# Kernel optimization log

Hardware: AMD Instinct MI355X
Metric: run time of the kernel (lower is better)

The kernel has to match this reference:

```python
import jax, jax.numpy as jnp
import numpy as np

N, D_IN, D_LAT, K = 65536, 1024, 128, 512


def setup_inputs() -> dict:
    key = jax.random.key(0)
    k1, k2, k3 = jax.random.split(key, 3)
    x = jax.random.normal(k1, (N, D_IN), dtype=jnp.float32)
    W = jax.random.normal(k2, (D_IN, D_LAT), dtype=jnp.float32) * 0.02
    b = jnp.zeros((D_LAT,), dtype=jnp.float32)
    centroids = jax.random.normal(k3, (K, D_LAT), dtype=jnp.float32)
    return {"x": x, "W": W, "b": b, "centroids": centroids}


def reference(x, W, b, centroids):
    alpha = 1.0
    # encoder: single linear layer -> latent l [N, D_LAT]
    l = x @ W + b
    # dist_to_centroids: vectorized squared-Euclidean cdist [N, K]
    # ||l - c||^2 = ||l||^2 + ||c||^2 - 2 l.c
    D = (jnp.sum(l * l, axis=1, keepdims=True)
         + jnp.sum(centroids * centroids, axis=1)
         - 2.0 * (l @ centroids.T))
    # Student's t-distribution kernel
    num = jnp.power(1.0 + D / alpha, -(alpha + 1.0) / 2.0)
    Q = num / jnp.sum(num, axis=1, keepdims=True)
    # target distribution
    Fq = jnp.sum(Q, axis=0)            # [K]
    num2 = (Q * Q) / Fq                # [N, K]
    P = num2 / jnp.sum(num2, axis=1, keepdims=True)
    return (l, Q, P)
```

## Files before the change

kernel.cpp:

```cpp
#include <hip/hip_runtime.h>

#define NROWS 65536
#define DIN   1024
#define DLAT  128
#define KC    512

typedef __attribute__((ext_vector_type(8))) short bf16x8;
typedef __attribute__((ext_vector_type(4))) float f32x4;

#define GLDS16(gp, lp)                                                          \
    __builtin_amdgcn_global_load_lds((const __attribute__((address_space(1))) void*)(gp), \
                                     (__attribute__((address_space(3))) void*)(lp), 16, 0, 0)

__device__ inline short f2bf(float f) {
    unsigned u = __float_as_uint(f);
    return (short)((u + 0x7FFFu + ((u >> 16) & 1u)) >> 16);
}

__global__ __launch_bounds__(256) void prep_convert(const float* __restrict__ W,
                                                    const float* __restrict__ C,
                                                    short* __restrict__ Wt,
                                                    short* __restrict__ cb) {
    int idx = blockIdx.x * 256 + threadIdx.x;
    if (idx < DLAT * DIN) {
        int n = idx >> 10, k = idx & 1023;
        Wt[idx] = f2bf(W[k * DLAT + n]);
    } else {
        int i2 = idx - DLAT * DIN;
        if (i2 < KC * DLAT) cb[i2] = f2bf(C[i2]);
    }
}

__global__ __launch_bounds__(64) void prep_csq(const float* __restrict__ C,
                                               float* __restrict__ csq) {
    int row = blockIdx.x;
    int lane = threadIdx.x;
    float a = C[row * DLAT + lane];
    float b = C[row * DLAT + 64 + lane];
    float s = a * a + b * b;
    #pragma unroll
    for (int m = 32; m >= 1; m >>= 1) s += __shfl_xor(s, m, 64);
    if (lane == 0) csq[row] = s;
}

__global__ __launch_bounds__(256, 2) void fused_aq(const float* __restrict__ x,
                                                   const short* __restrict__ Wt,
                                                   const float* __restrict__ bias,
                                                   const short* __restrict__ cb,
                                                   const float* __restrict__ csq,
                                                   float* __restrict__ lout,
                                                   float* __restrict__ Qout,
                                                   float* __restrict__ partial) {
    __shared__ char lds[65536];
    const int t = threadIdx.x;
    const int wid = t >> 6, lane = t & 63;
    const int l16 = lane & 15, lhi = lane >> 4;
    const int row0 = blockIdx.x * 64;

    const float* xsrc = x + (long)(row0 + (t >> 4)) * DIN + (((t & 15) ^ ((t >> 4) & 15)) << 2);
    const short* wsrc = Wt + (long)(t >> 3) * DIN + (((t & 7) ^ ((t >> 3) & 7)) << 3);
    const int lofs = t * 16;

    f32x4 acc[8];
    #pragma unroll
    for (int i = 0; i < 8; ++i) acc[i] = (f32x4){0.f, 0.f, 0.f, 0.f};

    {
        char* xb = lds;
        char* wb = lds + 16384;
        #pragma unroll
        for (int j = 0; j < 4; ++j) {
            GLDS16(xsrc + j * 16 * DIN, xb + lofs + j * 4096);
            GLDS16(wsrc + j * 32 * DIN, wb + lofs + j * 4096);
        }
    }
    __syncthreads();

    int cur = 0;
    const int arow = wid * 16 + l16;
    for (int kc = 0; kc < 16; ++kc) {
        if (kc < 15) {
            char* xb = lds + (cur ^ 1) * 32768;
            char* wb = xb + 16384;
            const float* xp = xsrc + (kc + 1) * 64;
            const short* wp = wsrc + (kc + 1) * 64;
            #pragma unroll
            for (int j = 0; j < 4; ++j) {
                GLDS16(xp + j * 16 * DIN, xb + lofs + j * 4096);
                GLDS16(wp + j * 32 * DIN, wb + lofs + j * 4096);
            }
        }
        const float* xs = (const float*)(lds + cur * 32768);
        const short* wl = (const short*)(lds + cur * 32768 + 16384);
        #pragma unroll
        for (int ks = 0; ks < 2; ++ks) {
            const int c4 = ks * 8 + lhi * 2;
            const float4 va0 = *(const float4*)(xs + arow * 64 + ((c4 ^ l16) << 2));
            const float4 va1 = *(const float4*)(xs + arow * 64 + (((c4 + 1) ^ l16) << 2));
            bf16x8 af;
            af[0] = f2bf(va0.x); af[1] = f2bf(va0.y); af[2] = f2bf(va0.z); af[3] = f2bf(va0.w);
            af[4] = f2bf(va1.x); af[5] = f2bf(va1.y); af[6] = f2bf(va1.z); af[7] = f2bf(va1.w);
            const int c8 = ks * 4 + lhi;
            #pragma unroll
            for (int nb = 0; nb < 8; ++nb) {
                const int n = nb * 16 + l16;
                const bf16x8 bf = *(const bf16x8*)(wl + n * 64 + ((c8 ^ (n & 7)) << 3));
                acc[nb] = __builtin_amdgcn_mfma_f32_16x16x32_bf16(af, bf, acc[nb], 0, 0, 0);
            }
        }
        __syncthreads();
        cur ^= 1;
    }

    float* l_lds = (float*)lds;
    #pragma unroll
    for (int nb = 0; nb < 8; ++nb) {
        const int col = nb * 16 + l16;
        const float bv = bias[col];
        const int slot = col >> 2, e = col & 3;
        #pragma unroll
        for (int r = 0; r < 4; ++r) {
            const int row = wid * 16 + lhi * 4 + r;
            const float v = acc[nb][r] + bv;
            lout[(long)(row0 + row) * DLAT + col] = v;
            l_lds[row * 128 + ((slot ^ (row & 15)) << 2) + e] = v;
        }
    }
    __syncthreads();

    float* lds_fq = (float*)(lds + 32768);
    const int row0w = row0 + wid * 16;

    bf16x8 af2[4];
    float sq = 0.f;
    #pragma unroll
    for (int ks = 0; ks < 4; ++ks) {
        const int s0 = 8 * ks + 2 * lhi;
        const float4 v0 = *(const float4*)(l_lds + arow * 128 + ((s0 ^ l16) << 2));
        const float4 v1 = *(const float4*)(l_lds + arow * 128 + (((s0 + 1) ^ l16) << 2));
        sq += v0.x * v0.x + v0.y * v0.y + v0.z * v0.z + v0.w * v0.w
            + v1.x * v1.x + v1.y * v1.y + v1.z * v1.z + v1.w * v1.w;
        bf16x8 a;
        a[0] = f2bf(v0.x); a[1] = f2bf(v0.y); a[2] = f2bf(v0.z); a[3] = f2bf(v0.w);
        a[4] = f2bf(v1.x); a[5] = f2bf(v1.y); a[6] = f2bf(v1.z); a[7] = f2bf(v1.w);
        af2[ks] = a;
    }
    sq += __shfl_xor(sq, 16, 64);
    sq += __shfl_xor(sq, 32, 64);
    float lsqr[4];
    #pragma unroll
    for (int r = 0; r < 4; ++r) lsqr[r] = __shfl(sq, lhi * 4 + r, 64);

    f32x4 numv[32];
    float rsum[4] = {0.f, 0.f, 0.f, 0.f};
    #pragma unroll
    for (int nb = 0; nb < 32; ++nb) {
        f32x4 s2 = (f32x4){0.f, 0.f, 0.f, 0.f};
        const short* cbase = cb + (nb * 16 + l16) * DLAT;
        #pragma unroll
        for (int ks = 0; ks < 4; ++ks) {
            const bf16x8 bf = *(const bf16x8*)(cbase + ks * 32 + lhi * 8);
            s2 = __builtin_amdgcn_mfma_f32_16x16x32_bf16(af2[ks], bf, s2, 0, 0, 0);
        }
        const float cs = csq[nb * 16 + l16];
        f32x4 nm;
        #pragma unroll
        for (int r = 0; r < 4; ++r) {
            float Dv = lsqr[r] + cs - 2.f * s2[r];
            float v = 1.f / (1.f + Dv);
            nm[r] = v;
            rsum[r] += v;
        }
        numv[nb] = nm;
    }
    #pragma unroll
    for (int m = 1; m <= 8; m <<= 1) {
        #pragma unroll
        for (int r = 0; r < 4; ++r) rsum[r] += __shfl_xor(rsum[r], m, 64);
    }
    float inv[4];
    #pragma unroll
    for (int r = 0; r < 4; ++r) inv[r] = 1.f / rsum[r];

    #pragma unroll
    for (int nb = 0; nb < 32; ++nb) {
        float cp = 0.f;
        #pragma unroll
        for (int r = 0; r < 4; ++r) {
            float q = numv[nb][r] * inv[r];
            Qout[(long)(row0w + lhi * 4 + r) * KC + nb * 16 + l16] = q;
            cp += q;
        }
        cp += __shfl_xor(cp, 16, 64);
        cp += __shfl_xor(cp, 32, 64);
        if (lhi == 0) lds_fq[wid * KC + nb * 16 + l16] = cp;
    }
    __syncthreads();
    for (int c = t; c < KC; c += 256) {
        partial[(long)blockIdx.x * KC + c] =
            lds_fq[0 * KC + c] + lds_fq[1 * KC + c] + lds_fq[2 * KC + c] + lds_fq[3 * KC + c];
    }
}

__global__ __launch_bounds__(256) void fq_reduce(const float* __restrict__ partial,
                                                 float* __restrict__ fqinv) {
    int c = blockIdx.x;
    float s = 0.f;
    #pragma unroll
    for (int i = 0; i < 4; ++i) s += partial[(long)(threadIdx.x + i * 256) * KC + c];
    __shared__ float red[256];
    red[threadIdx.x] = s;
    __syncthreads();
    for (int off = 128; off >= 1; off >>= 1) {
        if (threadIdx.x < off) red[threadIdx.x] += red[threadIdx.x + off];
        __syncthreads();
    }
    if (threadIdx.x == 0) fqinv[c] = 1.f / red[0];
}

__global__ __launch_bounds__(256, 2) void p_recompute(const float* __restrict__ lout,
                                                      const short* __restrict__ cb,
                                                      const float* __restrict__ csq,
                                                      const float* __restrict__ fqinv,
                                                      float* __restrict__ P) {
    const int wid = threadIdx.x >> 6, lane = threadIdx.x & 63;
    const int l16 = lane & 15, lhi = lane >> 4;
    const int row0 = blockIdx.x * 64 + wid * 16;

    bf16x8 af[4];
    float sq = 0.f;
    const float* lrow = lout + (long)(row0 + l16) * DLAT;
    #pragma unroll
    for (int ks = 0; ks < 4; ++ks) {
        const float4* lp = (const float4*)(lrow + ks * 32 + lhi * 8);
        float4 v0 = lp[0], v1 = lp[1];
        sq += v0.x * v0.x + v0.y * v0.y + v0.z * v0.z + v0.w * v0.w
            + v1.x * v1.x + v1.y * v1.y + v1.z * v1.z + v1.w * v1.w;
        bf16x8 a;
        a[0] = f2bf(v0.x); a[1] = f2bf(v0.y); a[2] = f2bf(v0.z); a[3] = f2bf(v0.w);
        a[4] = f2bf(v1.x); a[5] = f2bf(v1.y); a[6] = f2bf(v1.z); a[7] = f2bf(v1.w);
        af[ks] = a;
    }
    sq += __shfl_xor(sq, 16, 64);
    sq += __shfl_xor(sq, 32, 64);
    float lsqr[4];
    #pragma unroll
    for (int r = 0; r < 4; ++r) lsqr[r] = __shfl(sq, lhi * 4 + r, 64);

    f32x4 uv[32];
    float rsum[4] = {0.f, 0.f, 0.f, 0.f};
    #pragma unroll
    for (int nb = 0; nb < 32; ++nb) {
        f32x4 s2 = (f32x4){0.f, 0.f, 0.f, 0.f};
        const short* cbase = cb + (nb * 16 + l16) * DLAT;
        #pragma unroll
        for (int ks = 0; ks < 4; ++ks) {
            const bf16x8 bf = *(const bf16x8*)(cbase + ks * 32 + lhi * 8);
            s2 = __builtin_amdgcn_mfma_f32_16x16x32_bf16(af[ks], bf, s2, 0, 0, 0);
        }
        const float cs = csq[nb * 16 + l16];
        const float fqi = fqinv[nb * 16 + l16];
        f32x4 u;
        #pragma unroll
        for (int r = 0; r < 4; ++r) {
            float Dv = lsqr[r] + cs - 2.f * s2[r];
            float nm = 1.f / (1.f + Dv);
            float v = nm * nm * fqi;
            u[r] = v;
            rsum[r] += v;
        }
        uv[nb] = u;
    }
    #pragma unroll
    for (int m = 1; m <= 8; m <<= 1) {
        #pragma unroll
        for (int r = 0; r < 4; ++r) rsum[r] += __shfl_xor(rsum[r], m, 64);
    }
    float inv[4];
    #pragma unroll
    for (int r = 0; r < 4; ++r) inv[r] = 1.f / rsum[r];

    #pragma unroll
    for (int nb = 0; nb < 32; ++nb) {
        #pragma unroll
        for (int r = 0; r < 4; ++r) {
            P[(long)(row0 + lhi * 4 + r) * KC + nb * 16 + l16] = uv[nb][r] * inv[r];
        }
    }
}

extern "C" void kernel_launch(void* const* d_in, const int* in_sizes, int n_in,
                              void* d_out, int out_size, void* d_ws, size_t ws_size,
                              hipStream_t stream) {
    const float* x  = (const float*)d_in[0];
    const float* W  = (const float*)d_in[1];
    const float* b  = (const float*)d_in[2];
    const float* C  = (const float*)d_in[3];

    float* out  = (float*)d_out;
    float* lout = out;
    float* Qout = out + (long)NROWS * DLAT;
    float* Pout = Qout + (long)NROWS * KC;

    char*  ws      = (char*)d_ws;
    short* Wt      = (short*)ws;
    short* cb      = (short*)(ws + 262144);
    float* csq     = (float*)(ws + 262144 + 131072);
    float* partial = (float*)(ws + 395264);
    float* fqinv   = (float*)(ws + 395264 + 2097152);

    hipLaunchKernelGGL(prep_convert, dim3(768),  dim3(256), 0, stream, W, C, Wt, cb);
    hipLaunchKernelGGL(prep_csq,     dim3(512),  dim3(64),  0, stream, C, csq);
    hipLaunchKernelGGL(fused_aq,     dim3(1024), dim3(256), 0, stream,
                       x, Wt, b, cb, csq, lout, Qout, partial);
    hipLaunchKernelGGL(fq_reduce,    dim3(512),  dim3(256), 0, stream, partial, fqinv);
    hipLaunchKernelGGL(p_recompute,  dim3(1024), dim3(256), 0, stream,
                       lout, cb, csq, fqinv, Pout);
}
```

Measured before the change: 272.8 us.

## Coalesce Q/P/l stores via LDS staging, recompute distances, read W from global

The encoder GEMM now stages only x in LDS, using 128-wide K chunks over 8 iterations. W fragments are read straight from global/L2 instead of being double-buffered in LDS. The Q and P epilogues no longer keep 32 f32x4 numerators in registers. They recompute the distance MFMAs in two halves, write the results into a per-wave LDS buffer, and emit row-contiguous float4 stores, which also simplifies the column-sum reduction. This aims to cut register pressure and the strided 4-byte global stores, at the cost of doubling the distance MFMA work and adding uncached W loads in the main loop.

```diff
diff --git a/kernel.cpp b/kernel.cpp
--- a/kernel.cpp
+++ b/kernel.cpp
@@ -16,6 +16,8 @@
     unsigned u = __float_as_uint(f);
     return (short)((u + 0x7FFFu + ((u >> 16) & 1u)) >> 16);
 }
+
+#define MFMA __builtin_amdgcn_mfma_f32_16x16x32_bf16
 
 __global__ __launch_bounds__(256) void prep_convert(const float* __restrict__ W,
                                                     const float* __restrict__ C,
@@ -43,74 +45,60 @@
     if (lane == 0) csq[row] = s;
 }
 
-__global__ __launch_bounds__(256, 2) void fused_aq(const float* __restrict__ x,
-                                                   const short* __restrict__ Wt,
-                                                   const float* __restrict__ bias,
-                                                   const short* __restrict__ cb,
-                                                   const float* __restrict__ csq,
-                                                   float* __restrict__ lout,
-                                                   float* __restrict__ Qout,
-                                                   float* __restrict__ partial) {
+__global__ __launch_bounds__(256, 2) void fused2(const float* __restrict__ x,
+                                                 const short* __restrict__ Wt,
+                                                 const float* __restrict__ bias,
+                                                 const short* __restrict__ cb,
+                                                 const float* __restrict__ csq,
+                                                 float* __restrict__ lout,
+                                                 float* __restrict__ Qout,
+                                                 float* __restrict__ partial) {
     __shared__ char lds[65536];
     const int t = threadIdx.x;
     const int wid = t >> 6, lane = t & 63;
     const int l16 = lane & 15, lhi = lane >> 4;
     const int row0 = blockIdx.x * 64;
-
-    const float* xsrc = x + (long)(row0 + (t >> 4)) * DIN + (((t & 15) ^ ((t >> 4) & 15)) << 2);
-    const short* wsrc = Wt + (long)(t >> 3) * DIN + (((t & 7) ^ ((t >> 3) & 7)) << 3);
-    const int lofs = t * 16;
+    const int arow = wid * 16 + l16;
+
+    const int xrow_ = t >> 5, xslot = t & 31;
 
     f32x4 acc[8];
     #pragma unroll
     for (int i = 0; i < 8; ++i) acc[i] = (f32x4){0.f, 0.f, 0.f, 0.f};
 
-    {
-        char* xb = lds;
-        char* wb = lds + 16384;
-        #pragma unroll
-        for (int j = 0; j < 4; ++j) {
-            GLDS16(xsrc + j * 16 * DIN, xb + lofs + j * 4096);
-            GLDS16(wsrc + j * 32 * DIN, wb + lofs + j * 4096);
-        }
-    }
-    __syncthreads();
-
-    int cur = 0;
-    const int arow = wid * 16 + l16;
-    for (int kc = 0; kc < 16; ++kc) {
-        if (kc < 15) {
-            char* xb = lds + (cur ^ 1) * 32768;
-            char* wb = xb + 16384;
-            const float* xp = xsrc + (kc + 1) * 64;
-            const short* wp = wsrc + (kc + 1) * 64;
-            #pragma unroll
-            for (int j = 0; j < 4; ++j) {
-                GLDS16(xp + j * 16 * DIN, xb + lofs + j * 4096);
-                GLDS16(wp + j * 32 * DIN, wb + lofs + j * 4096);
-            }
-        }
-        const float* xs = (const float*)(lds + cur * 32768);
-        const short* wl = (const short*)(lds + cur * 32768 + 16384);
-        #pragma unroll
-        for (int ks = 0; ks < 2; ++ks) {
-            const int c4 = ks * 8 + lhi * 2;
-            const float4 va0 = *(const float4*)(xs + arow * 64 + ((c4 ^ l16) << 2));
-            const float4 va1 = *(const float4*)(xs + arow * 64 + (((c4 + 1) ^ l16) << 2));
+    #define XSTAGE(k, buf) {                                                         \
+        char* xb = lds + (buf) * 32768;                                              \
+        _Pragma("unroll")                                                            \
+        for (int j = 0; j < 8; ++j) {                                                \
+            const int row = j * 8 + xrow_;                                           \
+            GLDS16(x + (long)(row0 + row) * DIN + (k) * 128 + ((xslot ^ (row & 15)) << 2), \
+                   xb + (j * 256 + t) * 16);                                         \
+        } }
+
+    XSTAGE(0, 0);
+    __syncthreads();
+
+    for (int kc = 0; kc < 8; ++kc) {
+        if (kc < 7) XSTAGE(kc + 1, (kc + 1) & 1);
+        const float* xs = (const float*)(lds + (kc & 1) * 32768);
+        #pragma unroll
+        for (int ks = 0; ks < 4; ++ks) {
+            const int s0 = ks * 8 + lhi * 2;
+            const float4 va0 = *(const float4*)(xs + arow * 128 + (((s0    ) ^ l16) << 2));
+            const float4 va1 = *(const float4*)(xs + arow * 128 + (((s0 + 1) ^ l16) << 2));
             bf16x8 af;
             af[0] = f2bf(va0.x); af[1] = f2bf(va0.y); af[2] = f2bf(va0.z); af[3] = f2bf(va0.w);
             af[4] = f2bf(va1.x); af[5] = f2bf(va1.y); af[6] = f2bf(va1.z); af[7] = f2bf(va1.w);
-            const int c8 = ks * 4 + lhi;
             #pragma unroll
             for (int nb = 0; nb < 8; ++nb) {
-                const int n = nb * 16 + l16;
-                const bf16x8 bf = *(const bf16x8*)(wl + n * 64 + ((c8 ^ (n & 7)) << 3));
-                acc[nb] = __builtin_amdgcn_mfma_f32_16x16x32_bf16(af, bf, acc[nb], 0, 0, 0);
+                const bf16x8 bf = *(const bf16x8*)(Wt + (long)(nb * 16 + l16) * DIN
+                                                   + kc * 128 + ks * 32 + lhi * 8);
+                acc[nb] = MFMA(af, bf, acc[nb], 0, 0, 0);
             }
         }
         __syncthreads();
-        cur ^= 1;
-    }
+    }
+    #undef XSTAGE
 
     float* l_lds = (float*)lds;
     #pragma unroll
@@ -121,22 +109,23 @@
         #pragma unroll
         for (int r = 0; r < 4; ++r) {
             const int row = wid * 16 + lhi * 4 + r;
-            const float v = acc[nb][r] + bv;
-            lout[(long)(row0 + row) * DLAT + col] = v;
-            l_lds[row * 128 + ((slot ^ (row & 15)) << 2) + e] = v;
-        }
-    }
-    __syncthreads();
-
-    float* lds_fq = (float*)(lds + 32768);
-    const int row0w = row0 + wid * 16;
+            l_lds[row * 128 + ((slot ^ (row & 15)) << 2) + e] = acc[nb][r] + bv;
+        }
+    }
+    const int rsub = lane >> 5, c4l = lane & 31;
+    #pragma unroll
+    for (int it = 0; it < 8; ++it) {
+        const int row = wid * 16 + it * 2 + rsub;
+        const float4 v = *(const float4*)(l_lds + row * 128 + ((c4l ^ (row & 15)) << 2));
+        *(float4*)(lout + (long)(row0 + row) * DLAT + c4l * 4) = v;
+    }
 
     bf16x8 af2[4];
     float sq = 0.f;
     #pragma unroll
     for (int ks = 0; ks < 4; ++ks) {
-        const int s0 = 8 * ks + 2 * lhi;
-        const float4 v0 = *(const float4*)(l_lds + arow * 128 + ((s0 ^ l16) << 2));
+        const int s0 = ks * 8 + lhi * 2;
+        const float4 v0 = *(const float4*)(l_lds + arow * 128 + (((s0    ) ^ l16) << 2));
         const float4 v1 = *(const float4*)(l_lds + arow * 128 + (((s0 + 1) ^ l16) << 2));
         sq += v0.x * v0.x + v0.y * v0.y + v0.z * v0.z + v0.w * v0.w
             + v1.x * v1.x + v1.y * v1.y + v1.z * v1.z + v1.w * v1.w;
@@ -151,27 +140,18 @@
     #pragma unroll
     for (int r = 0; r < 4; ++r) lsqr[r] = __shfl(sq, lhi * 4 + r, 64);
 
-    f32x4 numv[32];
     float rsum[4] = {0.f, 0.f, 0.f, 0.f};
     #pragma unroll
     for (int nb = 0; nb < 32; ++nb) {
         f32x4 s2 = (f32x4){0.f, 0.f, 0.f, 0.f};
         const short* cbase = cb + (nb * 16 + l16) * DLAT;
         #pragma unroll
-        for (int ks = 0; ks < 4; ++ks) {
-            const bf16x8 bf = *(const bf16x8*)(cbase + ks * 32 + lhi * 8);
-            s2 = __builtin_amdgcn_mfma_f32_16x16x32_bf16(af2[ks], bf, s2, 0, 0, 0);
-        }
+        for (int ks = 0; ks < 4; ++ks)
+            s2 = MFMA(af2[ks], *(const bf16x8*)(cbase + ks * 32 + lhi * 8), s2, 0, 0, 0);
         const float cs = csq[nb * 16 + l16];
-        f32x4 nm;
-        #pragma unroll
-        for (int r = 0; r < 4; ++r) {
-            float Dv = lsqr[r] + cs - 2.f * s2[r];
-            float v = 1.f / (1.f + Dv);
-            nm[r] = v;
-            rsum[r] += v;
-        }
-        numv[nb] = nm;
+        #pragma unroll
+        for (int r = 0; r < 4; ++r)
+            rsum[r] += 1.f / (1.f + lsqr[r] + cs - 2.f * s2[r]);
     }
     #pragma unroll
     for (int m = 1; m <= 8; m <<= 1) {
@@ -182,18 +162,45 @@
     #pragma unroll
     for (int r = 0; r < 4; ++r) inv[r] = 1.f / rsum[r];
 
-    #pragma unroll
-    for (int nb = 0; nb < 32; ++nb) {
-        float cp = 0.f;
-        #pragma unroll
-        for (int r = 0; r < 4; ++r) {
-            float q = numv[nb][r] * inv[r];
-            Qout[(long)(row0w + lhi * 4 + r) * KC + nb * 16 + l16] = q;
-            cp += q;
-        }
-        cp += __shfl_xor(cp, 16, 64);
-        cp += __shfl_xor(cp, 32, 64);
-        if (lhi == 0) lds_fq[wid * KC + nb * 16 + l16] = cp;
+    __syncthreads();
+
+    float* wbuf = (float*)(lds + wid * 16384);
+    float cp4[4] = {0.f, 0.f, 0.f, 0.f};
+    #pragma unroll
+    for (int h = 0; h < 2; ++h) {
+        #pragma unroll
+        for (int nb = 0; nb < 32; ++nb) {
+            f32x4 s2 = (f32x4){0.f, 0.f, 0.f, 0.f};
+            const short* cbase = cb + (nb * 16 + l16) * DLAT;
+            #pragma unroll
+            for (int ks = 0; ks < 4; ++ks)
+                s2 = MFMA(af2[ks], *(const bf16x8*)(cbase + ks * 32 + lhi * 8), s2, 0, 0, 0);
+            const float cs = csq[nb * 16 + l16];
+            if ((lhi >> 1) == h) {
+                const int lr0 = (lhi & 1) * 4;
+                #pragma unroll
+                for (int r = 0; r < 4; ++r) {
+                    float nm = 1.f / (1.f + lsqr[r] + cs - 2.f * s2[r]);
+                    wbuf[(lr0 + r) * 512 + nb * 16 + l16] = nm * inv[r];
+                }
+            }
+        }
+        #pragma unroll
+        for (int it = 0; it < 4; ++it) {
+            const int lr = it * 2 + rsub;
+            const float4 v = *(const float4*)(wbuf + lr * 512 + c4l * 4);
+            *(float4*)(Qout + (long)(row0 + wid * 16 + h * 8 + lr) * KC + c4l * 4) = v;
+            cp4[0] += v.x; cp4[1] += v.y; cp4[2] += v.z; cp4[3] += v.w;
+        }
+    }
+    #pragma unroll
+    for (int i = 0; i < 4; ++i) cp4[i] += __shfl_xor(cp4[i], 32, 64);
+
+    __syncthreads();
+    float* lds_fq = (float*)lds;
+    if (lane < 32) {
+        float4 v = {cp4[0], cp4[1], cp4[2], cp4[3]};
+        *(float4*)(lds_fq + wid * KC + c4l * 4) = v;
     }
     __syncthreads();
     for (int c = t; c < KC; c += 256) {
@@ -218,28 +225,41 @@
     if (threadIdx.x == 0) fqinv[c] = 1.f / red[0];
 }
 
-__global__ __launch_bounds__(256, 2) void p_recompute(const float* __restrict__ lout,
-                                                      const short* __restrict__ cb,
-                                                      const float* __restrict__ csq,
-                                                      const float* __restrict__ fqinv,
-                                                      float* __restrict__ P) {
-    const int wid = threadIdx.x >> 6, lane = threadIdx.x & 63;
+__global__ __launch_bounds__(256, 2) void p2(const float* __restrict__ lout,
+                                             const short* __restrict__ cb,
+                                             const float* __restrict__ csq,
+                                             const float* __restrict__ fqinv,
+                                             float* __restrict__ P) {
+    __shared__ char lds[65536];
+    const int t = threadIdx.x;
+    const int wid = t >> 6, lane = t & 63;
     const int l16 = lane & 15, lhi = lane >> 4;
-    const int row0 = blockIdx.x * 64 + wid * 16;
-
-    bf16x8 af[4];
+    const int row0 = blockIdx.x * 64;
+    const int arow = wid * 16 + l16;
+    const int xrow_ = t >> 5, xslot = t & 31;
+
+    #pragma unroll
+    for (int j = 0; j < 8; ++j) {
+        const int row = j * 8 + xrow_;
+        GLDS16(lout + (long)(row0 + row) * DLAT + ((xslot ^ (row & 15)) << 2),
+               lds + (j * 256 + t) * 16);
+    }
+    __syncthreads();
+
+    float* l_lds = (float*)lds;
+    bf16x8 af2[4];
     float sq = 0.f;
-    const float* lrow = lout + (long)(row0 + l16) * DLAT;
     #pragma unroll
     for (int ks = 0; ks < 4; ++ks) {
-        const float4* lp = (const float4*)(lrow + ks * 32 + lhi * 8);
-        float4 v0 = lp[0], v1 = lp[1];
+        const int s0 = ks * 8 + lhi * 2;
+        const float4 v0 = *(const float4*)(l_lds + arow * 128 + (((s0    ) ^ l16) << 2));
+        const float4 v1 = *(const float4*)(l_lds + arow * 128 + (((s0 + 1) ^ l16) << 2));
         sq += v0.x * v0.x + v0.y * v0.y + v0.z * v0.z + v0.w * v0.w
             + v1.x * v1.x + v1.y * v1.y + v1.z * v1.z + v1.w * v1.w;
         bf16x8 a;
         a[0] = f2bf(v0.x); a[1] = f2bf(v0.y); a[2] = f2bf(v0.z); a[3] = f2bf(v0.w);
         a[4] = f2bf(v1.x); a[5] = f2bf(v1.y); a[6] = f2bf(v1.z); a[7] = f2bf(v1.w);
-        af[ks] = a;
+        af2[ks] = a;
     }
     sq += __shfl_xor(sq, 16, 64);
     sq += __shfl_xor(sq, 32, 64);
@@ -247,29 +267,21 @@
     #pragma unroll
     for (int r = 0; r < 4; ++r) lsqr[r] = __shfl(sq, lhi * 4 + r, 64);
 
-    f32x4 uv[32];
     float rsum[4] = {0.f, 0.f, 0.f, 0.f};
     #pragma unroll
     for (int nb = 0; nb < 32; ++nb) {
         f32x4 s2 = (f32x4){0.f, 0.f, 0.f, 0.f};
         const short* cbase = cb + (nb * 16 + l16) * DLAT;
         #pragma unroll
-        for (int ks = 0; ks < 4; ++ks) {
-            const bf16x8 bf = *(const bf16x8*)(cbase + ks * 32 + lhi * 8);
-            s2 = __builtin_amdgcn_mfma_f32_16x16x32_bf16(af[ks], bf, s2, 0, 0, 0);
-        }
+        for (int ks = 0; ks < 4; ++ks)
+            s2 = MFMA(af2[ks], *(const bf16x8*)(cbase + ks * 32 + lhi * 8), s2, 0, 0, 0);
         const float cs = csq[nb * 16 + l16];
         const float fqi = fqinv[nb * 16 + l16];
-        f32x4 u;
         #pragma unroll
         for (int r = 0; r < 4; ++r) {
-            float Dv = lsqr[r] + cs - 2.f * s2[r];
-            float nm = 1.f / (1.f + Dv);
-            float v = nm * nm * fqi;
-            u[r] = v;
-            rsum[r] += v;
-        }
-        uv[nb] = u;
+            float nm = 1.f / (1.f + lsqr[r] + cs - 2.f * s2[r]);
+            rsum[r] += nm * nm * fqi;
+        }
     }
     #pragma unroll
     for (int m = 1; m <= 8; m <<= 1) {
@@ -280,11 +292,35 @@
     #pragma unroll
     for (int r = 0; r < 4; ++r) inv[r] = 1.f / rsum[r];
 
-    #pragma unroll
-    for (int nb = 0; nb < 32; ++nb) {
-        #pragma unroll
-        for (int r = 0; r < 4; ++r) {
-            P[(long)(row0 + lhi * 4 + r) * KC + nb * 16 + l16] = uv[nb][r] * inv[r];
+    __syncthreads();
+
+    float* wbuf = (float*)(lds + wid * 16384);
+    const int rsub = lane >> 5, c4l = lane & 31;
+    #pragma unroll
+    for (int h = 0; h < 2; ++h) {
+        #pragma unroll
+        for (int nb = 0; nb < 32; ++nb) {
+            f32x4 s2 = (f32x4){0.f, 0.f, 0.f, 0.f};
+            const short* cbase = cb + (nb * 16 + l16) * DLAT;
+            #pragma unroll
+            for (int ks = 0; ks < 4; ++ks)
+                s2 = MFMA(af2[ks], *(const bf16x8*)(cbase + ks * 32 + lhi * 8), s2, 0, 0, 0);
+            const float cs = csq[nb * 16 + l16];
+            const float fqi = fqinv[nb * 16 + l16];
+            if ((lhi >> 1) == h) {
+                const int lr0 = (lhi & 1) * 4;
+                #pragma unroll
+                for (int r = 0; r < 4; ++r) {
+                    float nm = 1.f / (1.f + lsqr[r] + cs - 2.f * s2[r]);
+                    wbuf[(lr0 + r) * 512 + nb * 16 + l16] = nm * nm * fqi * inv[r];
+                }
+            }
+        }
+        #pragma unroll
+        for (int it = 0; it < 4; ++it) {
+            const int lr = it * 2 + rsub;
+            const float4 v = *(const float4*)(wbuf + lr * 512 + c4l * 4);
+            *(float4*)(P + (long)(row0 + wid * 16 + h * 8 + lr) * KC + c4l * 4) = v;
         }
     }
 }
@@ -311,9 +347,9 @@
 
     hipLaunchKernelGGL(prep_convert, dim3(768),  dim3(256), 0, stream, W, C, Wt, cb);
     hipLaunchKernelGGL(prep_csq,     dim3(512),  dim3(64),  0, stream, C, csq);
-    hipLaunchKernelGGL(fused_aq,     dim3(1024), dim3(256), 0, stream,
+    hipLaunchKernelGGL(fused2,       dim3(1024), dim3(256), 0, stream,
                        x, Wt, b, cb, csq, lout, Qout, partial);
     hipLaunchKernelGGL(fq_reduce,    dim3(512),  dim3(256), 0, stream, partial, fqinv);
-    hipLaunchKernelGGL(p_recompute,  dim3(1024), dim3(256), 0, stream,
+    hipLaunchKernelGGL(p2,           dim3(1024), dim3(256), 0, stream,
                        lout, cb, csq, fqinv, Pout);
 }
```

Result: slower. 692.7 us (+153.9%).
